# Optimization experiments

Hardware: AMD Instinct MI355X
Metric: run time of the kernel (lower is better)

Reference implementation:

```python
import jax, jax.numpy as jnp
import numpy as np

H = 2048
E = 8
K = 2
INTER = 2048
T = 2048


def setup_inputs() -> dict:
    key = jax.random.key(0)
    k1, k2, k3 = jax.random.split(key, 3)
    hidden_4d = jax.random.normal(k1, (1, 1, T, H), dtype=jnp.float32)
    # learned per-expert fused gate+up projection: [1, E, H, 2*inter]
    gate_up_proj = jax.random.normal(k2, (1, E, H, INTER * 2), dtype=jnp.float32) * 0.02
    # binary (expert, token) dispatch mask: on average K of E experts active per token
    sparsity = (jax.random.uniform(k3, (1, E, T, 1)) < (K / E)).astype(jnp.float32)
    return {"hidden_4d": hidden_4d, "gate_up_proj": gate_up_proj, "sparsity": sparsity}


def reference(hidden_4d, gate_up_proj, sparsity):
    # sparse_matmul semantics: per-expert GEMM of tokens against expert weight
    # blocks, with output blocks zeroed (skipped) where the sparsity mask is 0.
    # hidden_4d: [1, 1, T, H]; gate_up_proj: [1, E, H, F]; sparsity: [1, E, T, 1]
    # out[a, e, t, f] = mask[a, e, t] * sum_h hidden[a, 0, t, h] * W[a, e, h, f]
    out = jnp.einsum("abth,aehf->aetf", hidden_4d, gate_up_proj) * sparsity
    return out.sum()
```

## Files before the change

kernel.cpp:

```cpp
#include <hip/hip_runtime.h>

#define H_DIM 2048
#define E_DIM 8
#define T_DIM 2048
#define F_DIM 4096
#define NBLK  1024
#define HCHUNK 16

typedef float f32x4 __attribute__((ext_vector_type(4)));

__global__ __launch_bounds__(256, 4) void moe_dot(
    const float* __restrict__ hidden,
    const float* __restrict__ W,
    const float* __restrict__ mask,
    float* __restrict__ out) {
  const int tid = threadIdx.x;
  const int bid = blockIdx.x;
  const int e   = bid >> 7;
  const int h0  = (bid & 127) * HCHUNK;

  __shared__ float m_lds[T_DIM];
  __shared__ f32x4 redA[4][4];
  __shared__ float A_val[HCHUNK];
  __shared__ float wsum[4];

  {
    const f32x4* m4 = (const f32x4*)(mask + (size_t)e * T_DIM);
    f32x4* l4 = (f32x4*)m_lds;
    l4[tid]       = m4[tid];
    l4[tid + 256] = m4[tid + 256];
  }
  __syncthreads();

  const int hq   = tid & 3;
  const int ttg  = tid >> 2;
  const int wave = tid >> 6;
  const int lane = tid & 63;
  const int rl   = wave << 2;

  const float* hp = hidden + h0 + (hq << 2);
  const f32x4* rp = (const f32x4*)(W + ((size_t)e * H_DIM + h0 + rl) * F_DIM);

  f32x4 accA = (f32x4)0.f;
  f32x4 a0 = (f32x4)0.f, a1 = (f32x4)0.f, a2 = (f32x4)0.f, a3 = (f32x4)0.f;

  #pragma unroll
  for (int i = 0; i < 16; ++i) {
    int idx = lane + (i << 6);
    a0 += __builtin_nontemporal_load(&rp[idx]);
    a1 += __builtin_nontemporal_load(&rp[idx + 1024]);
    a2 += __builtin_nontemporal_load(&rp[idx + 2048]);
    a3 += __builtin_nontemporal_load(&rp[idx + 3072]);
    if (i < 8) {
      #pragma unroll
      for (int j = 0; j < 4; ++j) {
        int t = ttg + ((i * 4 + j) << 6);
        f32x4 hv = *(const f32x4*)(hp + (size_t)t * H_DIM);
        accA += hv * m_lds[t];
      }
    }
  }

  #pragma unroll
  for (int off = 4; off <= 32; off <<= 1) {
    accA.x += __shfl_down(accA.x, off, 64);
    accA.y += __shfl_down(accA.y, off, 64);
    accA.z += __shfl_down(accA.z, off, 64);
    accA.w += __shfl_down(accA.w, off, 64);
  }
  if (lane < 4) redA[wave][lane] = accA;
  __syncthreads();
  if (tid < 4)
    ((f32x4*)A_val)[tid] = (redA[0][tid] + redA[1][tid]) + (redA[2][tid] + redA[3][tid]);
  __syncthreads();

  float dot = ((a0.x + a0.y) + (a0.z + a0.w)) * A_val[rl]
            + ((a1.x + a1.y) + (a1.z + a1.w)) * A_val[rl + 1]
            + ((a2.x + a2.y) + (a2.z + a2.w)) * A_val[rl + 2]
            + ((a3.x + a3.y) + (a3.z + a3.w)) * A_val[rl + 3];

  #pragma unroll
  for (int off = 32; off > 0; off >>= 1)
    dot += __shfl_down(dot, off, 64);
  if (lane == 0) wsum[wave] = dot;
  __syncthreads();
  if (tid == 0)
    atomicAdd(out, (wsum[0] + wsum[1]) + (wsum[2] + wsum[3]));
}

extern "C" void kernel_launch(void* const* d_in, const int* in_sizes, int n_in,
                              void* d_out, int out_size, void* d_ws, size_t ws_size,
                              hipStream_t stream) {
  const float* hidden = (const float*)d_in[0];
  const float* W      = (const float*)d_in[1];
  const float* mask   = (const float*)d_in[2];
  float* out = (float*)d_out;

  hipMemsetAsync(d_out, 0, sizeof(float), stream);
  moe_dot<<<NBLK, 256, 0, stream>>>(hidden, W, mask, out);
}
```

Measured before the change: 427.2 us.

## Specialize one wave as producer for masked hidden sums, others stream weights

Splits each block's waves by role. One rotating wave loads the mask, computes the masked column sums of hidden, and reduces one weight row. The other three waves each reduce five weight rows without needing the hidden data. This removes the earlier cross-wave reduction and one barrier, and lets weight streaming overlap the hidden reduction. It also drops the nontemporal load hints. The producer wave now does 128 serial hidden loads on its own, which may become the critical path, and the per-wave work is unbalanced.

```diff
diff --git a/kernel.cpp b/kernel.cpp
--- a/kernel.cpp
+++ b/kernel.cpp
@@ -14,75 +14,91 @@
     const float* __restrict__ W,
     const float* __restrict__ mask,
     float* __restrict__ out) {
-  const int tid = threadIdx.x;
-  const int bid = blockIdx.x;
-  const int e   = bid >> 7;
-  const int h0  = (bid & 127) * HCHUNK;
+  const int tid  = threadIdx.x;
+  const int bid  = blockIdx.x;
+  const int e    = bid >> 7;
+  const int h0   = (bid & 127) * HCHUNK;
+  const int wave = tid >> 6;
+  const int lane = tid & 63;
 
   __shared__ float m_lds[T_DIM];
-  __shared__ f32x4 redA[4][4];
   __shared__ float A_val[HCHUNK];
   __shared__ float wsum[4];
 
-  {
+  const size_t wbase = ((size_t)e * H_DIM + h0) * F_DIM;
+  const int awave = bid & 3;
+  const bool producer = (wave == awave);
+
+  float sdot[5];
+  int r0 = 0;
+
+  if (producer) {
     const f32x4* m4 = (const f32x4*)(mask + (size_t)e * T_DIM);
     f32x4* l4 = (f32x4*)m_lds;
-    l4[tid]       = m4[tid];
-    l4[tid + 256] = m4[tid + 256];
-  }
-  __syncthreads();
+    #pragma unroll
+    for (int i = 0; i < 8; ++i) l4[lane + (i << 6)] = m4[lane + (i << 6)];
 
-  const int hq   = tid & 3;
-  const int ttg  = tid >> 2;
-  const int wave = tid >> 6;
-  const int lane = tid & 63;
-  const int rl   = wave << 2;
+    const int hq  = lane & 3;
+    const int ttg = lane >> 2;
+    const float* hp = hidden + h0 + (hq << 2);
+    f32x4 accA = (f32x4)0.f;
+    #pragma unroll 8
+    for (int k = 0; k < 128; ++k) {
+      int t = ttg + (k << 4);
+      accA += *(const f32x4*)(hp + (size_t)t * H_DIM) * m_lds[t];
+    }
+    #pragma unroll
+    for (int off = 4; off <= 32; off <<= 1) {
+      accA.x += __shfl_down(accA.x, off, 64);
+      accA.y += __shfl_down(accA.y, off, 64);
+      accA.z += __shfl_down(accA.z, off, 64);
+      accA.w += __shfl_down(accA.w, off, 64);
+    }
+    if (lane < 4) ((f32x4*)A_val)[lane] = accA;
 
-  const float* hp = hidden + h0 + (hq << 2);
-  const f32x4* rp = (const f32x4*)(W + ((size_t)e * H_DIM + h0 + rl) * F_DIM);
-
-  f32x4 accA = (f32x4)0.f;
-  f32x4 a0 = (f32x4)0.f, a1 = (f32x4)0.f, a2 = (f32x4)0.f, a3 = (f32x4)0.f;
-
-  #pragma unroll
-  for (int i = 0; i < 16; ++i) {
-    int idx = lane + (i << 6);
-    a0 += __builtin_nontemporal_load(&rp[idx]);
-    a1 += __builtin_nontemporal_load(&rp[idx + 1024]);
-    a2 += __builtin_nontemporal_load(&rp[idx + 2048]);
-    a3 += __builtin_nontemporal_load(&rp[idx + 3072]);
-    if (i < 8) {
-      #pragma unroll
-      for (int j = 0; j < 4; ++j) {
-        int t = ttg + ((i * 4 + j) << 6);
-        f32x4 hv = *(const f32x4*)(hp + (size_t)t * H_DIM);
-        accA += hv * m_lds[t];
-      }
+    const f32x4* rp = (const f32x4*)(W + wbase + (size_t)15 * F_DIM);
+    f32x4 a = (f32x4)0.f;
+    #pragma unroll 4
+    for (int i = 0; i < 16; ++i) a += rp[lane + (i << 6)];
+    float s = (a.x + a.y) + (a.z + a.w);
+    #pragma unroll
+    for (int off = 32; off > 0; off >>= 1) s += __shfl_down(s, off, 64);
+    if (lane == 0) wsum[wave] = s * A_val[15];
+  } else {
+    const int sw = wave - (wave > awave ? 1 : 0);
+    r0 = sw * 5;
+    const f32x4* rp = (const f32x4*)(W + wbase + (size_t)r0 * F_DIM);
+    f32x4 a0 = (f32x4)0.f, a1 = (f32x4)0.f, a2 = (f32x4)0.f,
+          a3 = (f32x4)0.f, a4 = (f32x4)0.f;
+    #pragma unroll 2
+    for (int i = 0; i < 16; ++i) {
+      int idx = lane + (i << 6);
+      a0 += rp[idx];
+      a1 += rp[idx + 1024];
+      a2 += rp[idx + 2048];
+      a3 += rp[idx + 3072];
+      a4 += rp[idx + 4096];
+    }
+    sdot[0] = (a0.x + a0.y) + (a0.z + a0.w);
+    sdot[1] = (a1.x + a1.y) + (a1.z + a1.w);
+    sdot[2] = (a2.x + a2.y) + (a2.z + a2.w);
+    sdot[3] = (a3.x + a3.y) + (a3.z + a3.w);
+    sdot[4] = (a4.x + a4.y) + (a4.z + a4.w);
+    #pragma unroll
+    for (int off = 32; off > 0; off >>= 1) {
+      sdot[0] += __shfl_down(sdot[0], off, 64);
+      sdot[1] += __shfl_down(sdot[1], off, 64);
+      sdot[2] += __shfl_down(sdot[2], off, 64);
+      sdot[3] += __shfl_down(sdot[3], off, 64);
+      sdot[4] += __shfl_down(sdot[4], off, 64);
     }
   }
 
-  #pragma unroll
-  for (int off = 4; off <= 32; off <<= 1) {
-    accA.x += __shfl_down(accA.x, off, 64);
-    accA.y += __shfl_down(accA.y, off, 64);
-    accA.z += __shfl_down(accA.z, off, 64);
-    accA.w += __shfl_down(accA.w, off, 64);
-  }
-  if (lane < 4) redA[wave][lane] = accA;
   __syncthreads();
-  if (tid < 4)
-    ((f32x4*)A_val)[tid] = (redA[0][tid] + redA[1][tid]) + (redA[2][tid] + redA[3][tid]);
-  __syncthreads();
-
-  float dot = ((a0.x + a0.y) + (a0.z + a0.w)) * A_val[rl]
-            + ((a1.x + a1.y) + (a1.z + a1.w)) * A_val[rl + 1]
-            + ((a2.x + a2.y) + (a2.z + a2.w)) * A_val[rl + 2]
-            + ((a3.x + a3.y) + (a3.z + a3.w)) * A_val[rl + 3];
-
-  #pragma unroll
-  for (int off = 32; off > 0; off >>= 1)
-    dot += __shfl_down(dot, off, 64);
-  if (lane == 0) wsum[wave] = dot;
+  if (!producer && lane == 0)
+    wsum[wave] = sdot[0] * A_val[r0]     + sdot[1] * A_val[r0 + 1]
+               + sdot[2] * A_val[r0 + 2] + sdot[3] * A_val[r0 + 3]
+               + sdot[4] * A_val[r0 + 4];
   __syncthreads();
   if (tid == 0)
     atomicAdd(out, (wsum[0] + wsum[1]) + (wsum[2] + wsum[3]));
```

Result: faster. 380.1 us (-11.0%).
